# Optimization experiments

Hardware: AMD Instinct MI355X
Metric: run time of the kernel (lower is better)

## Reference

```python
import jax, jax.numpy as jnp
import numpy as np

B, W, F = 64, 128, 64          # batch, window (node feat dim), n_features (nodes)
H, OUTW = 4, 128               # num_heads, out window size
NEG_SLOPE = 0.2                # LeakyReLU negative slope (alpha)


def setup_inputs() -> dict:
    key = jax.random.key(0)
    ks = jax.random.split(key, 6)
    scale_in = 1.0 / np.sqrt(W)
    scale_a = 1.0 / np.sqrt(OUTW)
    return {
        "x": jax.random.normal(ks[0], (B, W, F), dtype=jnp.float32),
        "W_src": jax.random.normal(ks[1], (H * OUTW, W), dtype=jnp.float32) * scale_in,
        "b_src": jnp.zeros((H * OUTW,), dtype=jnp.float32),
        "W_dst": jax.random.normal(ks[2], (H * OUTW, W), dtype=jnp.float32) * scale_in,
        "b_dst": jnp.zeros((H * OUTW,), dtype=jnp.float32),
        "attn": jax.random.normal(ks[3], (H, OUTW), dtype=jnp.float32) * scale_a,
    }


def reference(x, W_src, b_src, W_dst, b_dst, attn):
    # x: [B, W, F] -> node features nf: [B, F, W] (F nodes, W-dim features)
    nf = jnp.transpose(x, (0, 2, 1))
    b, f, w = nf.shape
    h, outw = attn.shape
    # GATv2 separate source/destination projections (share_weights=False)
    fs = (nf @ W_src.T + b_src).reshape(b, f, h, outw)  # [B, F, H, outW]
    fd = (nf @ W_dst.T + b_dst).reshape(b, f, h, outw)
    # additive score over complete graph with self-loops: e[b,i,j,h,d]
    s = fs[:, :, None, :, :] + fd[:, None, :, :, :]      # [B, src, dst, H, outW]
    e = jnp.where(s >= 0, s, NEG_SLOPE * s)              # LeakyReLU
    scores = jnp.einsum('bijhd,hd->bhij', e, attn)       # [B, H, src, dst]
    # edge softmax: normalize over incoming edges (sources) per destination
    a = jax.nn.softmax(scores, axis=2)
    # weighted scatter-sum aggregation at destinations
    out = jnp.einsum('bhij,bihd->bjhd', a, fs)           # [B, F, H, outW]
    out = out.mean(axis=2)                               # mean over heads -> [B, F, outW]
    return jnp.transpose(out, (0, 2, 1))                 # [B, outW, F]
```

## Files before the change

kernel.cpp:

```cpp
#include <hip/hip_runtime.h>
#include <math.h>

#define BB 64
#define WW 128
#define FF 64
#define HH 4
#define OW 128


struct GemmRegion {
    float xq[64 * 64];
    float wq[2 * 128 * 68];
};
struct AttnRegion {
    float fsl[FF * 132];
    float fdl[FF * 132];
    float st[FF * 68];
    float A6[OW], B4[OW];
    float redm[16 * 64];
    float reds[16 * 64];
};
union SMem { GemmRegion g; AttnRegion a; };

__global__ __launch_bounds__(1024) void gat_fused(
    const float* __restrict__ x,
    const float* __restrict__ Wsrc,
    const float* __restrict__ bsrc,
    const float* __restrict__ Wdst,
    const float* __restrict__ bdst,
    const float* __restrict__ attn,
    float* __restrict__ out)
{
    __shared__ __align__(16) SMem sm;
    __shared__ float bl[2 * 128];

    const int bx = blockIdx.x;
    const int h  = bx & 3;
    const int b  = bx >> 2;
    const int t  = threadIdx.x;

    const int m  = t >> 9;
    const int i0 = (t & 15) * 4;
    const int g2 = (t >> 4) & 31;
    const int d0 = (g2 >> 2) * 16 + (g2 & 3) * 4;

    if (t < 256) bl[t] = (t & 128 ? bdst : bsrc)[h * 128 + (t & 127)];

    float acc[4][4] = {};

    for (int kh = 0; kh < 2; ++kh) {
        if (kh) __syncthreads();
        {
            const int k = t >> 4, iq = t & 15;
            *(float4*)&sm.g.xq[k * 64 + iq * 4] =
                *(const float4*)(x + ((size_t)b * WW + kh * 64 + k) * FF + iq * 4);
        }
        #pragma unroll
        for (int p = 0; p < 4; ++p) {
            const int idx = p * 1024 + t;
            const int mm = idx >> 11, d = (idx >> 4) & 127, q = idx & 15;
            *(float4*)&sm.g.wq[(mm * 128 + d) * 68 + q * 4] =
                *(const float4*)((mm ? Wdst : Wsrc)
                                 + (size_t)(h * 128 + d) * WW + kh * 64 + q * 4);
        }
        __syncthreads();

        #pragma unroll 4
        for (int k0 = 0; k0 < 64; k0 += 4) {
            float4 xv[4], wv[4];
            #pragma unroll
            for (int kk = 0; kk < 4; ++kk)
                xv[kk] = *(const float4*)&sm.g.xq[(k0 + kk) * 64 + i0];
            #pragma unroll
            for (int e = 0; e < 4; ++e)
                wv[e] = *(const float4*)&sm.g.wq[(m * 128 + d0 + e) * 68 + k0];
            #pragma unroll
            for (int kk = 0; kk < 4; ++kk) {
                #pragma unroll
                for (int e = 0; e < 4; ++e) {
                    const float wf = ((const float*)&wv[e])[kk];
                    const float* xf = (const float*)&xv[kk];
                    acc[e][0] = fmaf(xf[0], wf, acc[e][0]);
                    acc[e][1] = fmaf(xf[1], wf, acc[e][1]);
                    acc[e][2] = fmaf(xf[2], wf, acc[e][2]);
                    acc[e][3] = fmaf(xf[3], wf, acc[e][3]);
                }
            }
        }
    }
    __syncthreads();

    {
        float* dst = m ? sm.a.fdl : sm.a.fsl;
        const float b0 = bl[m * 128 + d0 + 0];
        const float b1 = bl[m * 128 + d0 + 1];
        const float b2 = bl[m * 128 + d0 + 2];
        const float b3 = bl[m * 128 + d0 + 3];
        #pragma unroll
        for (int ii = 0; ii < 4; ++ii) {
            float4 o;
            o.x = acc[0][ii] + b0;
            o.y = acc[1][ii] + b1;
            o.z = acc[2][ii] + b2;
            o.w = acc[3][ii] + b3;
            *(float4*)&dst[(i0 + ii) * 132 + d0] = o;
        }
        if (t < 128) {
            const float av = attn[h * OW + t];
            sm.a.A6[t] = 0.6f * av;
            sm.a.B4[t] = 0.4f * av;
        }
    }
    __syncthreads();

    if (t < 256) {
        const int i = t & 63, sel = t >> 6;
        const float* src = (sel < 2 ? sm.a.fsl : sm.a.fdl) + i * 132 + (sel & 1) * 64;
        const float* a6  = sm.a.A6 + (sel & 1) * 64;
        float s = 0.0f;
        #pragma unroll
        for (int c = 0; c < 16; ++c) {
            float4 fv = *(const float4*)&src[c * 4];
            float4 av = *(const float4*)&a6[c * 4];
            s = fmaf(fv.x, av.x, fmaf(fv.y, av.y, fmaf(fv.z, av.z, fmaf(fv.w, av.w, s))));
        }
        sm.a.redm[sel * 64 + i] = s;
    }
    __syncthreads();

    {
        const int lane = t & 63;
        const int jl0  = (t >> 6) * 4;
        float sc[4] = {};
        #pragma unroll 8
        for (int c = 0; c < 32; ++c) {
            const int dd0 = c * 4;
            float4 fsv = *(const float4*)&sm.a.fsl[lane * 132 + dd0];
            float4 b4  = *(const float4*)&sm.a.B4[dd0];
            #pragma unroll
            for (int jj = 0; jj < 4; ++jj) {
                float4 fdv = *(const float4*)&sm.a.fdl[(jl0 + jj) * 132 + dd0];
                float r = sc[jj];
                r = fmaf(b4.x, fabsf(fsv.x + fdv.x), r);
                r = fmaf(b4.y, fabsf(fsv.y + fdv.y), r);
                r = fmaf(b4.z, fabsf(fsv.z + fdv.z), r);
                r = fmaf(b4.w, fabsf(fsv.w + fdv.w), r);
                sc[jj] = r;
            }
        }
        const float csl = sm.a.redm[lane] + sm.a.redm[64 + lane];
        float4 o;
        o.x = sc[0] + csl + sm.a.redm[128 + jl0 + 0] + sm.a.redm[192 + jl0 + 0];
        o.y = sc[1] + csl + sm.a.redm[128 + jl0 + 1] + sm.a.redm[192 + jl0 + 1];
        o.z = sc[2] + csl + sm.a.redm[128 + jl0 + 2] + sm.a.redm[192 + jl0 + 2];
        o.w = sc[3] + csl + sm.a.redm[128 + jl0 + 3] + sm.a.redm[192 + jl0 + 3];
        *(float4*)&sm.a.st[lane * 68 + jl0] = o;
    }
    __syncthreads();

    {
        const int j = t & 63, s = t >> 6;
        const int i0s = s * 4;
        float mx = sm.a.st[i0s * 68 + j];
        #pragma unroll
        for (int k = 1; k < 4; ++k) mx = fmaxf(mx, sm.a.st[(i0s + k) * 68 + j]);
        sm.a.redm[s * 64 + j] = mx;
    }
    __syncthreads();
    {
        const int j = t & 63, s = t >> 6;
        const int i0s = s * 4;
        float mj = sm.a.redm[j];
        #pragma unroll
        for (int s2 = 1; s2 < 16; ++s2) mj = fmaxf(mj, sm.a.redm[s2 * 64 + j]);
        float ps = 0.0f;
        #pragma unroll
        for (int k = 0; k < 4; ++k) {
            float e = __expf(sm.a.st[(i0s + k) * 68 + j] - mj);
            sm.a.st[(i0s + k) * 68 + j] = e;
            ps += e;
        }
        sm.a.reds[s * 64 + j] = ps;
    }
    __syncthreads();

    {
        const int j = t & 63, dblk = t >> 6;
        float l = 0.0f;
        #pragma unroll
        for (int s2 = 0; s2 < 16; ++s2) l += sm.a.reds[s2 * 64 + j];
        const float iv = 0.25f / l;

        float ag[8] = {};
        #pragma unroll 4
        for (int i = 0; i < FF; ++i) {
            const float p = sm.a.st[i * 68 + j];
            const float* fr = &sm.a.fsl[i * 132 + dblk * 8];
            float4 f0 = *(const float4*)(fr);
            float4 f1 = *(const float4*)(fr + 4);
            ag[0] = fmaf(p, f0.x, ag[0]);  ag[1] = fmaf(p, f0.y, ag[1]);
            ag[2] = fmaf(p, f0.z, ag[2]);  ag[3] = fmaf(p, f0.w, ag[3]);
            ag[4] = fmaf(p, f1.x, ag[4]);  ag[5] = fmaf(p, f1.y, ag[5]);
            ag[6] = fmaf(p, f1.z, ag[6]);  ag[7] = fmaf(p, f1.w, ag[7]);
        }
        float* ob = out + ((size_t)b * OW + dblk * 8) * FF + j;
        #pragma unroll
        for (int e = 0; e < 8; ++e)
            atomicAdd(ob + e * FF, ag[e] * iv);
    }
}

extern "C" void kernel_launch(void* const* d_in, const int* in_sizes, int n_in,
                              void* d_out, int out_size, void* d_ws, size_t ws_size,
                              hipStream_t stream) {
    const float* x    = (const float*)d_in[0];
    const float* Wsrc = (const float*)d_in[1];
    const float* bsrc = (const float*)d_in[2];
    const float* Wdst = (const float*)d_in[3];
    const float* bdst = (const float*)d_in[4];
    const float* attn = (const float*)d_in[5];

    hipMemsetAsync(d_out, 0, (size_t)out_size, stream);
    gat_fused<<<BB * HH, 1024, 0, stream>>>(x, Wsrc, bsrc, Wdst, bdst, attn,
                                            (float*)d_out);
}
```

Before: 105.1 us.

## Coarsen per-thread tiles in projection, score and aggregation phases

The projection GEMM now runs on 256 threads, each computing an 8x8 register tile instead of a 4x4 tile on all 1024 threads. The score and aggregation phases run on 512 threads, each handling twice as many destination columns or output dims. The aim is more register reuse per shared-memory load and fewer LDS reads overall. The cost is that most of the 1024-thread block sits idle in these phases. The new `__launch_bounds__(1024, 4)` hint may also cap VGPRs tightly enough to cause spills with the larger accumulator arrays.

```diff
diff --git a/kernel.cpp b/kernel.cpp
--- a/kernel.cpp
+++ b/kernel.cpp
@@ -22,7 +22,7 @@
 };
 union SMem { GemmRegion g; AttnRegion a; };
 
-__global__ __launch_bounds__(1024) void gat_fused(
+__global__ __launch_bounds__(1024, 4) void gat_fused(
     const float* __restrict__ x,
     const float* __restrict__ Wsrc,
     const float* __restrict__ bsrc,
@@ -39,14 +39,14 @@
     const int b  = bx >> 2;
     const int t  = threadIdx.x;
 
-    const int m  = t >> 9;
-    const int i0 = (t & 15) * 4;
-    const int g2 = (t >> 4) & 31;
-    const int d0 = (g2 >> 2) * 16 + (g2 & 3) * 4;
+    const int m  = t >> 7;
+    const int ig = (t >> 4) & 7;
+    const int dg = t & 15;
+    const int i0 = ig * 8;
 
     if (t < 256) bl[t] = (t & 128 ? bdst : bsrc)[h * 128 + (t & 127)];
 
-    float acc[4][4] = {};
+    float acc[8][8] = {};
 
     for (int kh = 0; kh < 2; ++kh) {
         if (kh) __syncthreads();
@@ -65,51 +65,54 @@
         }
         __syncthreads();
 
-        #pragma unroll 4
-        for (int k0 = 0; k0 < 64; k0 += 4) {
-            float4 xv[4], wv[4];
-            #pragma unroll
-            for (int kk = 0; kk < 4; ++kk)
-                xv[kk] = *(const float4*)&sm.g.xq[(k0 + kk) * 64 + i0];
-            #pragma unroll
-            for (int e = 0; e < 4; ++e)
-                wv[e] = *(const float4*)&sm.g.wq[(m * 128 + d0 + e) * 68 + k0];
-            #pragma unroll
-            for (int kk = 0; kk < 4; ++kk) {
+        if (t < 256) {
+            #pragma unroll 2
+            for (int k0 = 0; k0 < 64; k0 += 4) {
+                float4 xv[8];
                 #pragma unroll
-                for (int e = 0; e < 4; ++e) {
-                    const float wf = ((const float*)&wv[e])[kk];
-                    const float* xf = (const float*)&xv[kk];
-                    acc[e][0] = fmaf(xf[0], wf, acc[e][0]);
-                    acc[e][1] = fmaf(xf[1], wf, acc[e][1]);
-                    acc[e][2] = fmaf(xf[2], wf, acc[e][2]);
-                    acc[e][3] = fmaf(xf[3], wf, acc[e][3]);
+                for (int kk = 0; kk < 4; ++kk) {
+                    xv[kk * 2 + 0] = *(const float4*)&sm.g.xq[(k0 + kk) * 64 + i0];
+                    xv[kk * 2 + 1] = *(const float4*)&sm.g.xq[(k0 + kk) * 64 + i0 + 4];
+                }
+                #pragma unroll
+                for (int e = 0; e < 8; ++e) {
+                    const float4 wv =
+                        *(const float4*)&sm.g.wq[(m * 128 + dg + 16 * e) * 68 + k0];
+                    #pragma unroll
+                    for (int kk = 0; kk < 4; ++kk) {
+                        const float wf = ((const float*)&wv)[kk];
+                        const float* xa = (const float*)&xv[kk * 2];
+                        const float* xb = (const float*)&xv[kk * 2 + 1];
+                        acc[0][e] = fmaf(xa[0], wf, acc[0][e]);
+                        acc[1][e] = fmaf(xa[1], wf, acc[1][e]);
+                        acc[2][e] = fmaf(xa[2], wf, acc[2][e]);
+                        acc[3][e] = fmaf(xa[3], wf, acc[3][e]);
+                        acc[4][e] = fmaf(xb[0], wf, acc[4][e]);
+                        acc[5][e] = fmaf(xb[1], wf, acc[5][e]);
+                        acc[6][e] = fmaf(xb[2], wf, acc[6][e]);
+                        acc[7][e] = fmaf(xb[3], wf, acc[7][e]);
+                    }
                 }
             }
         }
     }
     __syncthreads();
 
-    {
+    if (t < 256) {
         float* dst = m ? sm.a.fdl : sm.a.fsl;
-        const float b0 = bl[m * 128 + d0 + 0];
-        const float b1 = bl[m * 128 + d0 + 1];
-        const float b2 = bl[m * 128 + d0 + 2];
-        const float b3 = bl[m * 128 + d0 + 3];
-        #pragma unroll
-        for (int ii = 0; ii < 4; ++ii) {
-            float4 o;
-            o.x = acc[0][ii] + b0;
-            o.y = acc[1][ii] + b1;
-            o.z = acc[2][ii] + b2;
-            o.w = acc[3][ii] + b3;
-            *(float4*)&dst[(i0 + ii) * 132 + d0] = o;
-        }
-        if (t < 128) {
-            const float av = attn[h * OW + t];
-            sm.a.A6[t] = 0.6f * av;
-            sm.a.B4[t] = 0.4f * av;
-        }
+        #pragma unroll
+        for (int e = 0; e < 8; ++e) {
+            const int d = dg + 16 * e;
+            const float bv = bl[m * 128 + d];
+            #pragma unroll
+            for (int ii = 0; ii < 8; ++ii)
+                dst[(i0 + ii) * 132 + d] = acc[ii][e] + bv;
+        }
+    }
+    if (t < 128) {
+        const float av = attn[h * OW + t];
+        sm.a.A6[t] = 0.6f * av;
+        sm.a.B4[t] = 0.4f * av;
     }
     __syncthreads();
 
@@ -128,17 +131,17 @@
     }
     __syncthreads();
 
-    {
+    if (t < 512) {
         const int lane = t & 63;
-        const int jl0  = (t >> 6) * 4;
-        float sc[4] = {};
-        #pragma unroll 8
+        const int jl0  = (t >> 6) * 8;
+        float sc[8] = {};
+        #pragma unroll 4
         for (int c = 0; c < 32; ++c) {
             const int dd0 = c * 4;
             float4 fsv = *(const float4*)&sm.a.fsl[lane * 132 + dd0];
             float4 b4  = *(const float4*)&sm.a.B4[dd0];
             #pragma unroll
-            for (int jj = 0; jj < 4; ++jj) {
+            for (int jj = 0; jj < 8; ++jj) {
                 float4 fdv = *(const float4*)&sm.a.fdl[(jl0 + jj) * 132 + dd0];
                 float r = sc[jj];
                 r = fmaf(b4.x, fabsf(fsv.x + fdv.x), r);
@@ -149,12 +152,17 @@
             }
         }
         const float csl = sm.a.redm[lane] + sm.a.redm[64 + lane];
-        float4 o;
-        o.x = sc[0] + csl + sm.a.redm[128 + jl0 + 0] + sm.a.redm[192 + jl0 + 0];
-        o.y = sc[1] + csl + sm.a.redm[128 + jl0 + 1] + sm.a.redm[192 + jl0 + 1];
-        o.z = sc[2] + csl + sm.a.redm[128 + jl0 + 2] + sm.a.redm[192 + jl0 + 2];
-        o.w = sc[3] + csl + sm.a.redm[128 + jl0 + 3] + sm.a.redm[192 + jl0 + 3];
-        *(float4*)&sm.a.st[lane * 68 + jl0] = o;
+        float4 o0, o1;
+        o0.x = sc[0] + csl + sm.a.redm[128 + jl0 + 0] + sm.a.redm[192 + jl0 + 0];
+        o0.y = sc[1] + csl + sm.a.redm[128 + jl0 + 1] + sm.a.redm[192 + jl0 + 1];
+        o0.z = sc[2] + csl + sm.a.redm[128 + jl0 + 2] + sm.a.redm[192 + jl0 + 2];
+        o0.w = sc[3] + csl + sm.a.redm[128 + jl0 + 3] + sm.a.redm[192 + jl0 + 3];
+        o1.x = sc[4] + csl + sm.a.redm[128 + jl0 + 4] + sm.a.redm[192 + jl0 + 4];
+        o1.y = sc[5] + csl + sm.a.redm[128 + jl0 + 5] + sm.a.redm[192 + jl0 + 5];
+        o1.z = sc[6] + csl + sm.a.redm[128 + jl0 + 6] + sm.a.redm[192 + jl0 + 6];
+        o1.w = sc[7] + csl + sm.a.redm[128 + jl0 + 7] + sm.a.redm[192 + jl0 + 7];
+        *(float4*)&sm.a.st[lane * 68 + jl0]     = o0;
+        *(float4*)&sm.a.st[lane * 68 + jl0 + 4] = o1;
     }
     __syncthreads();
 
@@ -184,28 +192,34 @@
     }
     __syncthreads();
 
-    {
+    if (t < 512) {
         const int j = t & 63, dblk = t >> 6;
         float l = 0.0f;
         #pragma unroll
         for (int s2 = 0; s2 < 16; ++s2) l += sm.a.reds[s2 * 64 + j];
         const float iv = 0.25f / l;
 
-        float ag[8] = {};
+        float ag[16] = {};
         #pragma unroll 4
         for (int i = 0; i < FF; ++i) {
             const float p = sm.a.st[i * 68 + j];
-            const float* fr = &sm.a.fsl[i * 132 + dblk * 8];
+            const float* fr = &sm.a.fsl[i * 132 + dblk * 16];
             float4 f0 = *(const float4*)(fr);
             float4 f1 = *(const float4*)(fr + 4);
-            ag[0] = fmaf(p, f0.x, ag[0]);  ag[1] = fmaf(p, f0.y, ag[1]);
-            ag[2] = fmaf(p, f0.z, ag[2]);  ag[3] = fmaf(p, f0.w, ag[3]);
-            ag[4] = fmaf(p, f1.x, ag[4]);  ag[5] = fmaf(p, f1.y, ag[5]);
-            ag[6] = fmaf(p, f1.z, ag[6]);  ag[7] = fmaf(p, f1.w, ag[7]);
-        }
-        float* ob = out + ((size_t)b * OW + dblk * 8) * FF + j;
-        #pragma unroll
-        for (int e = 0; e < 8; ++e)
+            float4 f2 = *(const float4*)(fr + 8);
+            float4 f3 = *(const float4*)(fr + 12);
+            ag[0]  = fmaf(p, f0.x, ag[0]);  ag[1]  = fmaf(p, f0.y, ag[1]);
+            ag[2]  = fmaf(p, f0.z, ag[2]);  ag[3]  = fmaf(p, f0.w, ag[3]);
+            ag[4]  = fmaf(p, f1.x, ag[4]);  ag[5]  = fmaf(p, f1.y, ag[5]);
+            ag[6]  = fmaf(p, f1.z, ag[6]);  ag[7]  = fmaf(p, f1.w, ag[7]);
+            ag[8]  = fmaf(p, f2.x, ag[8]);  ag[9]  = fmaf(p, f2.y, ag[9]);
+            ag[10] = fmaf(p, f2.z, ag[10]); ag[11] = fmaf(p, f2.w, ag[11]);
+            ag[12] = fmaf(p, f3.x, ag[12]); ag[13] = fmaf(p, f3.y, ag[13]);
+            ag[14] = fmaf(p, f3.z, ag[14]); ag[15] = fmaf(p, f3.w, ag[15]);
+        }
+        float* ob = out + ((size_t)b * OW + dblk * 16) * FF + j;
+        #pragma unroll
+        for (int e = 0; e < 16; ++e)
             atomicAdd(ob + e * FF, ag[e] * iv);
     }
 }
```

Result: slower. 112.6 us (+7.1%).
